# Kernel optimization log

Measured on AMD Instinct MI355X. Metric: run time of the kernel, lower is better.

## Reference

```python
import jax, jax.numpy as jnp
import numpy as np
import math

B, T, N, D = 2, 128, 64, 128
H = 8
DK = D // H
DE = 32
LW = 8
CLIP_MIN, CLIP_MAX = -5.0, 5.0


def setup_inputs() -> dict:
    key = jax.random.key(0)
    ks = jax.random.split(key, 12)
    node = jax.random.normal(ks[0], (B, T, N, D), jnp.float32)
    tv = jax.random.normal(ks[1], (B, N, T, T, DE), jnp.float32)
    mask = jax.random.randint(ks[2], (B, 1, T), 0, 2, jnp.int32)
    # banded local mask |i-j| <= LW
    idx = jnp.arange(T)
    local_mask = (jnp.abs(idx[:, None] - idx[None, :]) <= LW).astype(jnp.float32)
    s = 0.02
    W_qkv = jax.random.normal(ks[3], (D, 3 * D), jnp.float32) * s
    b_qkv = jnp.zeros((3 * D,), jnp.float32)
    W_g = jax.random.normal(ks[4], (DE, H), jnp.float32) * s
    b_g = jnp.zeros((H,), jnp.float32)
    W_out = jax.random.normal(ks[5], (D, D), jnp.float32) * s
    b_out = jnp.zeros((D,), jnp.float32)
    W_upd = jax.random.normal(ks[6], (H, DE), jnp.float32) * s
    b_upd = jnp.zeros((DE,), jnp.float32)
    return {"node": node, "tv": tv, "mask": mask, "local_mask": local_mask,
            "W_qkv": W_qkv, "b_qkv": b_qkv, "W_g": W_g, "b_g": b_g,
            "W_out": W_out, "b_out": b_out, "W_upd": W_upd, "b_upd": b_upd}


def reference(node, tv, mask, local_mask, W_qkv, b_qkv, W_g, b_g, W_out, b_out, W_upd, b_upd):
    # node: (B,T,N,D) -> (B*N, T, D)  (einops '(b n) t d' ordering: index b*N+n)
    x = node.transpose(0, 2, 1, 3).reshape(B * N, T, D)
    qkv = x @ W_qkv + b_qkv                              # (BN, T, 3D)
    qkv = qkv.reshape(B * N, T, H, DK, 3)                # grouped (h, d_k, 3)
    q = qkv[..., 0].transpose(0, 2, 1, 3)                # (BN, H, T, DK)
    k = qkv[..., 1].transpose(0, 2, 1, 3)
    v = qkv[..., 2].transpose(0, 2, 1, 3)
    # edge-conditioned bias g: (BN, T, T, DE) -> (BN, H, T, T)
    g = (tv.reshape(B * N, T, T, DE) @ W_g + b_g).transpose(0, 3, 1, 2)
    scores = jnp.einsum('bhtd,bhsd->bhts', q, k) / math.sqrt(DK)
    scores = scores + g * local_mask                     # banded edge bias
    scores = jnp.clip(scores, CLIP_MIN, CLIP_MAX)
    m = jnp.repeat(mask, N, axis=0)[:, None]             # (BN,1,1,T)
    scores = jnp.where(m == 0, jnp.float32(1e-28), scores)
    attn = jax.nn.softmax(scores, axis=-1)
    attn = jnp.where(m == 0, jnp.float32(0.0), attn)
    xo = jnp.einsum('bhts,bhsd->bhtd', attn, v)          # (BN,H,T,DK)
    xo = xo.transpose(0, 2, 1, 3).reshape(B, N, T, D).transpose(0, 2, 1, 3)  # (B,T,N,D)
    xo = xo @ W_out + b_out
    sc = scores.reshape(B, N, H, T, T).transpose(0, 1, 3, 4, 2)  # (B,N,T,T,H)
    tv_out = sc @ W_upd + b_upd                          # (B,N,T,T,DE)
    return (xo, tv_out)
```

## Files before the change

### kernel.cpp

```cpp
#include <hip/hip_runtime.h>
#include <math.h>

#define BB 2
#define TT 128
#define NN 64
#define DD 128
#define HH 8
#define DKK 16
#define DEE 32
#define LWW 8
#define BNN (BB*NN)

typedef float floatx4 __attribute__((ext_vector_type(4)));

__global__ __launch_bounds__(256) void qkv_kernel(
    const float* __restrict__ node, const float* __restrict__ Wqkv,
    const float* __restrict__ bqkv,
    float* __restrict__ Q, float* __restrict__ K, float* __restrict__ V) {
  __shared__ float xs[32 * 128];
  __shared__ float wl[16 * 384];
  const int tid = threadIdx.x;
  const int row0 = blockIdx.x * 32;

  for (int i4 = tid; i4 < 1024; i4 += 256) {
    int r = i4 >> 5, d4 = i4 & 31;
    int rowg = row0 + r;
    int bn = rowg >> 7, t = rowg & 127;
    int b = bn >> 6, n = bn & 63;
    float4 v = *(const float4*)&node[(((size_t)(b * TT + t)) * NN + n) * DD + d4 * 4];
    *(float4*)&xs[r * 128 + d4 * 4] = v;
  }

  float acc[48];
#pragma unroll
  for (int i = 0; i < 48; ++i) acc[i] = 0.f;
  const int tr = tid >> 5;
  const int tc = tid & 31;

  for (int ct = 0; ct < 8; ++ct) {
    __syncthreads();
    for (int i4 = tid; i4 < 1536; i4 += 256) {
      int c = i4 / 96, j4 = i4 % 96;
      *(float4*)&wl[c * 384 + j4 * 4] =
          *(const float4*)&Wqkv[(size_t)(ct * 16 + c) * 384 + j4 * 4];
    }
    __syncthreads();
#pragma unroll
    for (int cl4 = 0; cl4 < 4; ++cl4) {
      floatx4 xr[4];
#pragma unroll
      for (int i = 0; i < 4; ++i)
        xr[i] = *(const floatx4*)&xs[(tr * 4 + i) * 128 + ct * 16 + cl4 * 4];
#pragma unroll
      for (int jj = 0; jj < 4; ++jj) {
        const float* wp = &wl[(cl4 * 4 + jj) * 384 + tc * 12];
        floatx4 w0 = *(const floatx4*)&wp[0];
        floatx4 w1 = *(const floatx4*)&wp[4];
        floatx4 w2 = *(const floatx4*)&wp[8];
#pragma unroll
        for (int i = 0; i < 4; ++i) {
          float x = xr[i][jj];
          acc[i * 12 + 0] += x * w0[0];  acc[i * 12 + 1] += x * w0[1];
          acc[i * 12 + 2] += x * w0[2];  acc[i * 12 + 3] += x * w0[3];
          acc[i * 12 + 4] += x * w1[0];  acc[i * 12 + 5] += x * w1[1];
          acc[i * 12 + 6] += x * w1[2];  acc[i * 12 + 7] += x * w1[3];
          acc[i * 12 + 8] += x * w2[0];  acc[i * 12 + 9] += x * w2[1];
          acc[i * 12 +10] += x * w2[2];  acc[i * 12 +11] += x * w2[3];
        }
      }
    }
  }

  const int h = tc >> 2;
  const int dk0 = (tc & 3) * 4;
#pragma unroll
  for (int i = 0; i < 4; ++i) {
    int rowg = row0 + tr * 4 + i;
    int bn = rowg >> 7, t = rowg & 127;
    float qv[4], kv[4], vv[4];
#pragma unroll
    for (int dl = 0; dl < 4; ++dl) {
      int jb = h * 48 + (dk0 + dl) * 3;
      qv[dl] = acc[i * 12 + dl * 3 + 0] + bqkv[jb + 0];
      kv[dl] = acc[i * 12 + dl * 3 + 1] + bqkv[jb + 1];
      vv[dl] = acc[i * 12 + dl * 3 + 2] + bqkv[jb + 2];
    }
    *(float4*)&Q[(size_t)rowg * 128 + h * 16 + dk0] = *(float4*)qv;
    *(float4*)&K[(((size_t)(bn * 8 + h)) * 128 + t) * 16 + dk0] = *(float4*)kv;
#pragma unroll
    for (int dl = 0; dl < 4; ++dl)
      V[(((size_t)(bn * 8 + h)) * 16 + dk0 + dl) * 128 + t] = vv[dl];
  }
}

__global__ __launch_bounds__(256) void attn_kernel(
    const float* __restrict__ Q, const float* __restrict__ K,
    const float* __restrict__ V, const float* __restrict__ tv,
    const int* __restrict__ mask,
    const float* __restrict__ Wg, const float* __restrict__ bg,
    const float* __restrict__ Wout, const float* __restrict__ bout,
    const float* __restrict__ Wupd, const float* __restrict__ bupd,
    float* __restrict__ out0, float* __restrict__ out1) {
  __shared__ float sc[8 * 8 * 128];
  __shared__ float qs[8 * 128];
  __shared__ float swg[DEE * HH];
  __shared__ float swu[HH * DEE];
  __shared__ float sbg[HH];
  __shared__ float sbu[DEE];
  __shared__ int smask[TT];

  const int tid = threadIdx.x;
  const int xcd = blockIdx.x & 7;
  const int i = blockIdx.x >> 3;
  const int bn = xcd * 16 + (i & 15);
  const int t0 = (i >> 4) * 8;
  const int b = bn >> 6, n = bn & 63;

  swg[tid & 255] = Wg[tid & 255];
  swu[tid & 255] = Wupd[tid & 255];
  if (tid < DEE) sbu[tid] = bupd[tid];
  if (tid < HH) sbg[tid] = bg[tid];
  if (tid < TT) smask[tid] = mask[b * TT + tid];
  __syncthreads();

  {
    const int h = tid >> 5;
    const int s4 = tid & 31;
    const floatx4* kp =
        (const floatx4*)&K[(((size_t)(bn * 8 + h)) * 128 + s4 * 4) * 16];
    floatx4 kr[16];
#pragma unroll
    for (int u = 0; u < 16; ++u) kr[u] = kp[u];
    int m[4];
#pragma unroll
    for (int j = 0; j < 4; ++j) m[j] = smask[s4 * 4 + j];
#pragma unroll
    for (int t8 = 0; t8 < 8; ++t8) {
      const floatx4* qp =
          (const floatx4*)&Q[((size_t)(bn * TT + t0 + t8)) * 128 + h * 16];
      floatx4 q0 = qp[0], q1 = qp[1], q2 = qp[2], q3 = qp[3];
      const int t = t0 + t8;
      floatx4 res;
#pragma unroll
      for (int j = 0; j < 4; ++j) {
        floatx4 p = q0 * kr[j * 4 + 0];
        p += q1 * kr[j * 4 + 1];
        p += q2 * kr[j * 4 + 2];
        p += q3 * kr[j * 4 + 3];
        float v = (p[0] + p[1] + p[2] + p[3]) * 0.25f;
        int s = s4 * 4 + j;
        bool inband = (s >= t - LWW) && (s <= t + LWW);
        if (!inband) {
          v = fminf(fmaxf(v, -5.f), 5.f);
          if (m[j] == 0) v = 1e-28f;
        }
        res[j] = v;
      }
      *(floatx4*)&sc[(t8 * 8 + h) * 128 + s4 * 4] = res;
    }
  }
  __syncthreads();

  if (tid < 8 * (2 * LWW + 1)) {
    int t8 = tid / 17, ds = tid % 17;
    int t = t0 + t8, s = t - LWW + ds;
    if (s >= 0 && s < TT) {
      const float4* tp = (const float4*)&tv[(((size_t)(bn * TT + t)) * TT + s) * DEE];
      float gh[HH];
#pragma unroll
      for (int h = 0; h < HH; ++h) gh[h] = sbg[h];
#pragma unroll
      for (int c4 = 0; c4 < 8; ++c4) {
        float4 tvv = tp[c4];
#pragma unroll
        for (int h = 0; h < HH; ++h) {
          gh[h] += tvv.x * swg[(c4 * 4 + 0) * 8 + h] +
                   tvv.y * swg[(c4 * 4 + 1) * 8 + h] +
                   tvv.z * swg[(c4 * 4 + 2) * 8 + h] +
                   tvv.w * swg[(c4 * 4 + 3) * 8 + h];
        }
      }
      int m0 = smask[s];
#pragma unroll
      for (int h = 0; h < HH; ++h) {
        float v = sc[(t8 * 8 + h) * 128 + s] + gh[h];
        v = fminf(fmaxf(v, -5.f), 5.f);
        if (m0 == 0) v = 1e-28f;
        sc[(t8 * 8 + h) * 128 + s] = v;
      }
    }
  }
  __syncthreads();

  {
    const int e4 = tid & 7;
    const int sq = tid >> 3;
    floatx4 wv[HH];
#pragma unroll
    for (int h = 0; h < HH; ++h) wv[h] = *(const floatx4*)&swu[h * 32 + e4 * 4];
    floatx4 bu = *(const floatx4*)&sbu[e4 * 4];
    for (int t8 = 0; t8 < 8; ++t8) {
      float* op = out1 + (((size_t)(bn * TT + t0 + t8)) * TT) * DEE;
      floatx4 o0 = bu, o1 = bu, o2 = bu, o3 = bu;
#pragma unroll
      for (int h = 0; h < HH; ++h) {
        floatx4 f = *(const floatx4*)&sc[(t8 * 8 + h) * 128 + sq * 4];
        o0 += f[0] * wv[h];
        o1 += f[1] * wv[h];
        o2 += f[2] * wv[h];
        o3 += f[3] * wv[h];
      }
      __builtin_nontemporal_store(o0, (floatx4*)&op[(sq * 4 + 0) * DEE + e4 * 4]);
      __builtin_nontemporal_store(o1, (floatx4*)&op[(sq * 4 + 1) * DEE + e4 * 4]);
      __builtin_nontemporal_store(o2, (floatx4*)&op[(sq * 4 + 2) * DEE + e4 * 4]);
      __builtin_nontemporal_store(o3, (floatx4*)&op[(sq * 4 + 3) * DEE + e4 * 4]);
    }
  }
  __syncthreads();

  {
    const int l = tid & 31;
    const int rsub = tid >> 5;
#pragma unroll
    for (int p = 0; p < 8; ++p) {
      int row = p * 8 + rsub;
      float* r = &sc[row * 128];
      float x0 = r[l], x1 = r[l + 32], x2 = r[l + 64], x3 = r[l + 96];
      float m = fmaxf(fmaxf(x0, x1), fmaxf(x2, x3));
      m = fmaxf(m, __shfl_xor(m, 1));
      m = fmaxf(m, __shfl_xor(m, 2));
      m = fmaxf(m, __shfl_xor(m, 4));
      m = fmaxf(m, __shfl_xor(m, 8));
      m = fmaxf(m, __shfl_xor(m, 16));
      float e0 = __expf(x0 - m), e1 = __expf(x1 - m),
            e2 = __expf(x2 - m), e3 = __expf(x3 - m);
      float ssum = e0 + e1 + e2 + e3;
      ssum += __shfl_xor(ssum, 1);
      ssum += __shfl_xor(ssum, 2);
      ssum += __shfl_xor(ssum, 4);
      ssum += __shfl_xor(ssum, 8);
      ssum += __shfl_xor(ssum, 16);
      float inv = 1.f / ssum;
      r[l]      = (smask[l]      == 0) ? 0.f : e0 * inv;
      r[l + 32] = (smask[l + 32] == 0) ? 0.f : e1 * inv;
      r[l + 64] = (smask[l + 64] == 0) ? 0.f : e2 * inv;
      r[l + 96] = (smask[l + 96] == 0) ? 0.f : e3 * inv;
    }
  }
  __syncthreads();

  {
    const int dk4 = tid & 3;
    const int h = (tid >> 2) & 7;
    const int t8 = tid >> 5;
    const int rr = (t8 * 8 + h) & 31;
    const floatx4* ap = (const floatx4*)&sc[(t8 * 8 + h) * 128];
    const floatx4* vp0 =
        (const floatx4*)&V[(((size_t)(bn * 8 + h)) * 16 + dk4 * 4 + 0) * 128];
    const floatx4* vp1 =
        (const floatx4*)&V[(((size_t)(bn * 8 + h)) * 16 + dk4 * 4 + 1) * 128];
    const floatx4* vp2 =
        (const floatx4*)&V[(((size_t)(bn * 8 + h)) * 16 + dk4 * 4 + 2) * 128];
    const floatx4* vp3 =
        (const floatx4*)&V[(((size_t)(bn * 8 + h)) * 16 + dk4 * 4 + 3) * 128];
    floatx4 a0 = 0.f, a1 = 0.f, a2 = 0.f, a3 = 0.f;
#pragma unroll 8
    for (int it = 0; it < 32; ++it) {
      int s4 = (it + rr) & 31;
      floatx4 av = ap[s4];
      a0 += av * vp0[s4];
      a1 += av * vp1[s4];
      a2 += av * vp2[s4];
      a3 += av * vp3[s4];
    }
    floatx4 r;
    r[0] = a0[0] + a0[1] + a0[2] + a0[3];
    r[1] = a1[0] + a1[1] + a1[2] + a1[3];
    r[2] = a2[0] + a2[1] + a2[2] + a2[3];
    r[3] = a3[0] + a3[1] + a3[2] + a3[3];
    *(floatx4*)&qs[t8 * 128 + h * 16 + dk4 * 4] = r;
  }
  __syncthreads();

  {
    const int d = tid & 127, tg = tid >> 7;
    float bo = bout[d];
    float accp[4] = {bo, bo, bo, bo};
    for (int c4 = 0; c4 < 32; ++c4) {
      floatx4 x0 = *(const floatx4*)&qs[(tg * 4 + 0) * 128 + c4 * 4];
      floatx4 x1 = *(const floatx4*)&qs[(tg * 4 + 1) * 128 + c4 * 4];
      floatx4 x2 = *(const floatx4*)&qs[(tg * 4 + 2) * 128 + c4 * 4];
      floatx4 x3 = *(const floatx4*)&qs[(tg * 4 + 3) * 128 + c4 * 4];
      const float* wp = &Wout[(size_t)(c4 * 4) * 128 + d];
      float w0 = wp[0], w1 = wp[128], w2 = wp[256], w3 = wp[384];
      accp[0] += x0[0] * w0 + x0[1] * w1 + x0[2] * w2 + x0[3] * w3;
      accp[1] += x1[0] * w0 + x1[1] * w1 + x1[2] * w2 + x1[3] * w3;
      accp[2] += x2[0] * w0 + x2[1] * w1 + x2[2] * w2 + x2[3] * w3;
      accp[3] += x3[0] * w0 + x3[1] * w1 + x3[2] * w2 + x3[3] * w3;
    }
#pragma unroll
    for (int u = 0; u < 4; ++u) {
      int t = t0 + tg * 4 + u;
      __builtin_nontemporal_store(accp[u],
          &out0[(((size_t)(b * TT + t)) * NN + n) * DD + d]);
    }
  }
}

extern "C" void kernel_launch(void* const* d_in, const int* in_sizes, int n_in,
                              void* d_out, int out_size, void* d_ws, size_t ws_size,
                              hipStream_t stream) {
  const float* node = (const float*)d_in[0];
  const float* tv   = (const float*)d_in[1];
  const int*   mask = (const int*)d_in[2];
  const float* Wqkv = (const float*)d_in[4];
  const float* bqkv = (const float*)d_in[5];
  const float* Wg   = (const float*)d_in[6];
  const float* bg   = (const float*)d_in[7];
  const float* Wout = (const float*)d_in[8];
  const float* bout = (const float*)d_in[9];
  const float* Wupd = (const float*)d_in[10];
  const float* bupd = (const float*)d_in[11];

  float* out0 = (float*)d_out;
  float* out1 = out0 + (size_t)BB * TT * NN * DD;

  float* Q = (float*)d_ws;
  float* K = Q + (size_t)BNN * TT * DD;
  float* V = K + (size_t)BNN * TT * DD;

  qkv_kernel<<<512, 256, 0, stream>>>(node, Wqkv, bqkv, Q, K, V);
  attn_kernel<<<2048, 256, 0, stream>>>(Q, K, V, tv, mask, Wg, bg, Wout, bout,
                                        Wupd, bupd, out0, out1);
}
```

Before: 636.8 us.

## Make attention stages wave-local and halve QKV tile rows

The attention kernel now gives each 64-lane wave two query rows for every stage after score computation, so block-wide __syncthreads become wave barriers. Shared copies of the small weights and the mask are dropped in favour of direct global loads. The score buffer gets a padded stride to avoid LDS bank conflicts, and the output projection uses vectorized Wout loads with a cross-half shuffle reduction. The QKV kernel processes 16 rows per block and launches twice as many blocks, trading weight-tile reuse for more parallelism and fewer registers.

```diff
diff --git a/kernel.cpp b/kernel.cpp
--- a/kernel.cpp
+++ b/kernel.cpp
@@ -10,6 +10,7 @@
 #define DEE 32
 #define LWW 8
 #define BNN (BB*NN)
+#define SCP 132
 
 typedef float floatx4 __attribute__((ext_vector_type(4)));
 
@@ -17,23 +18,23 @@
     const float* __restrict__ node, const float* __restrict__ Wqkv,
     const float* __restrict__ bqkv,
     float* __restrict__ Q, float* __restrict__ K, float* __restrict__ V) {
-  __shared__ float xs[32 * 128];
+  __shared__ float xs[16 * 128];
   __shared__ float wl[16 * 384];
   const int tid = threadIdx.x;
-  const int row0 = blockIdx.x * 32;
-
-  for (int i4 = tid; i4 < 1024; i4 += 256) {
+  const int row0 = blockIdx.x * 16;
+
+  for (int i4 = tid; i4 < 512; i4 += 256) {
     int r = i4 >> 5, d4 = i4 & 31;
     int rowg = row0 + r;
     int bn = rowg >> 7, t = rowg & 127;
     int b = bn >> 6, n = bn & 63;
-    float4 v = *(const float4*)&node[(((size_t)(b * TT + t)) * NN + n) * DD + d4 * 4];
-    *(float4*)&xs[r * 128 + d4 * 4] = v;
-  }
-
-  float acc[48];
-#pragma unroll
-  for (int i = 0; i < 48; ++i) acc[i] = 0.f;
+    *(float4*)&xs[r * 128 + d4 * 4] =
+        *(const float4*)&node[(((size_t)(b * TT + t)) * NN + n) * DD + d4 * 4];
+  }
+
+  float acc[24];
+#pragma unroll
+  for (int i = 0; i < 24; ++i) acc[i] = 0.f;
   const int tr = tid >> 5;
   const int tc = tid & 31;
 
@@ -47,10 +48,10 @@
     __syncthreads();
 #pragma unroll
     for (int cl4 = 0; cl4 < 4; ++cl4) {
-      floatx4 xr[4];
-#pragma unroll
-      for (int i = 0; i < 4; ++i)
-        xr[i] = *(const floatx4*)&xs[(tr * 4 + i) * 128 + ct * 16 + cl4 * 4];
+      floatx4 xr[2];
+#pragma unroll
+      for (int i = 0; i < 2; ++i)
+        xr[i] = *(const floatx4*)&xs[(tr * 2 + i) * 128 + ct * 16 + cl4 * 4];
 #pragma unroll
       for (int jj = 0; jj < 4; ++jj) {
         const float* wp = &wl[(cl4 * 4 + jj) * 384 + tc * 12];
@@ -58,7 +59,7 @@
         floatx4 w1 = *(const floatx4*)&wp[4];
         floatx4 w2 = *(const floatx4*)&wp[8];
 #pragma unroll
-        for (int i = 0; i < 4; ++i) {
+        for (int i = 0; i < 2; ++i) {
           float x = xr[i][jj];
           acc[i * 12 + 0] += x * w0[0];  acc[i * 12 + 1] += x * w0[1];
           acc[i * 12 + 2] += x * w0[2];  acc[i * 12 + 3] += x * w0[3];
@@ -74,8 +75,8 @@
   const int h = tc >> 2;
   const int dk0 = (tc & 3) * 4;
 #pragma unroll
-  for (int i = 0; i < 4; ++i) {
-    int rowg = row0 + tr * 4 + i;
+  for (int i = 0; i < 2; ++i) {
+    int rowg = row0 + tr * 2 + i;
     int bn = rowg >> 7, t = rowg & 127;
     float qv[4], kv[4], vv[4];
 #pragma unroll
@@ -101,13 +102,8 @@
     const float* __restrict__ Wout, const float* __restrict__ bout,
     const float* __restrict__ Wupd, const float* __restrict__ bupd,
     float* __restrict__ out0, float* __restrict__ out1) {
-  __shared__ float sc[8 * 8 * 128];
-  __shared__ float qs[8 * 128];
-  __shared__ float swg[DEE * HH];
-  __shared__ float swu[HH * DEE];
-  __shared__ float sbg[HH];
-  __shared__ float sbu[DEE];
-  __shared__ int smask[TT];
+  __shared__ float sc[64 * SCP];
+  __shared__ float xo[4][2][128];
 
   const int tid = threadIdx.x;
   const int xcd = blockIdx.x & 7;
@@ -116,13 +112,6 @@
   const int t0 = (i >> 4) * 8;
   const int b = bn >> 6, n = bn & 63;
 
-  swg[tid & 255] = Wg[tid & 255];
-  swu[tid & 255] = Wupd[tid & 255];
-  if (tid < DEE) sbu[tid] = bupd[tid];
-  if (tid < HH) sbg[tid] = bg[tid];
-  if (tid < TT) smask[tid] = mask[b * TT + tid];
-  __syncthreads();
-
   {
     const int h = tid >> 5;
     const int s4 = tid & 31;
@@ -131,9 +120,8 @@
     floatx4 kr[16];
 #pragma unroll
     for (int u = 0; u < 16; ++u) kr[u] = kp[u];
-    int m[4];
-#pragma unroll
-    for (int j = 0; j < 4; ++j) m[j] = smask[s4 * 4 + j];
+    int4 mi = *(const int4*)&mask[b * TT + s4 * 4];
+    int m[4] = {mi.x, mi.y, mi.z, mi.w};
 #pragma unroll
     for (int t8 = 0; t8 < 8; ++t8) {
       const floatx4* qp =
@@ -156,154 +144,187 @@
         }
         res[j] = v;
       }
-      *(floatx4*)&sc[(t8 * 8 + h) * 128 + s4 * 4] = res;
+      *(floatx4*)&sc[(t8 * 8 + h) * SCP + s4 * 4] = res;
     }
   }
   __syncthreads();
 
-  if (tid < 8 * (2 * LWW + 1)) {
-    int t8 = tid / 17, ds = tid % 17;
-    int t = t0 + t8, s = t - LWW + ds;
+  const int wid = tid >> 6, lane = tid & 63;
+  const int tw0 = t0 + wid * 2;
+  float* scw = &sc[(wid * 2) * 8 * SCP];
+
+  if (lane < 34) {
+    const int r = lane / 17, ds = lane - r * 17;
+    const int t = tw0 + r, s = t - LWW + ds;
     if (s >= 0 && s < TT) {
-      const float4* tp = (const float4*)&tv[(((size_t)(bn * TT + t)) * TT + s) * DEE];
-      float gh[HH];
-#pragma unroll
-      for (int h = 0; h < HH; ++h) gh[h] = sbg[h];
+      const floatx4* tp =
+          (const floatx4*)&tv[(((size_t)(bn * TT + t)) * TT + s) * DEE];
+      floatx4 glo = *(const floatx4*)&bg[0];
+      floatx4 ghi = *(const floatx4*)&bg[4];
 #pragma unroll
       for (int c4 = 0; c4 < 8; ++c4) {
-        float4 tvv = tp[c4];
-#pragma unroll
-        for (int h = 0; h < HH; ++h) {
-          gh[h] += tvv.x * swg[(c4 * 4 + 0) * 8 + h] +
-                   tvv.y * swg[(c4 * 4 + 1) * 8 + h] +
-                   tvv.z * swg[(c4 * 4 + 2) * 8 + h] +
-                   tvv.w * swg[(c4 * 4 + 3) * 8 + h];
+        floatx4 tvv = tp[c4];
+#pragma unroll
+        for (int k = 0; k < 4; ++k) {
+          floatx4 wlo = *(const floatx4*)&Wg[(c4 * 4 + k) * 8];
+          floatx4 whi = *(const floatx4*)&Wg[(c4 * 4 + k) * 8 + 4];
+          glo += tvv[k] * wlo;
+          ghi += tvv[k] * whi;
         }
       }
-      int m0 = smask[s];
-#pragma unroll
-      for (int h = 0; h < HH; ++h) {
-        float v = sc[(t8 * 8 + h) * 128 + s] + gh[h];
+      int m0 = mask[b * TT + s];
+      float* base = &scw[r * 8 * SCP + s];
+#pragma unroll
+      for (int h = 0; h < 8; ++h) {
+        float gv = (h < 4) ? glo[h] : ghi[h - 4];
+        float v = base[h * SCP] + gv;
         v = fminf(fmaxf(v, -5.f), 5.f);
         if (m0 == 0) v = 1e-28f;
-        sc[(t8 * 8 + h) * 128 + s] = v;
-      }
-    }
-  }
-  __syncthreads();
-
-  {
-    const int e4 = tid & 7;
-    const int sq = tid >> 3;
+        base[h * SCP] = v;
+      }
+    }
+  }
+  __builtin_amdgcn_wave_barrier();
+
+  {
+    const int e4 = lane & 7;
+    const int sq0 = lane >> 3;
     floatx4 wv[HH];
 #pragma unroll
-    for (int h = 0; h < HH; ++h) wv[h] = *(const floatx4*)&swu[h * 32 + e4 * 4];
-    floatx4 bu = *(const floatx4*)&sbu[e4 * 4];
-    for (int t8 = 0; t8 < 8; ++t8) {
-      float* op = out1 + (((size_t)(bn * TT + t0 + t8)) * TT) * DEE;
-      floatx4 o0 = bu, o1 = bu, o2 = bu, o3 = bu;
-#pragma unroll
-      for (int h = 0; h < HH; ++h) {
-        floatx4 f = *(const floatx4*)&sc[(t8 * 8 + h) * 128 + sq * 4];
-        o0 += f[0] * wv[h];
-        o1 += f[1] * wv[h];
-        o2 += f[2] * wv[h];
-        o3 += f[3] * wv[h];
-      }
-      __builtin_nontemporal_store(o0, (floatx4*)&op[(sq * 4 + 0) * DEE + e4 * 4]);
-      __builtin_nontemporal_store(o1, (floatx4*)&op[(sq * 4 + 1) * DEE + e4 * 4]);
-      __builtin_nontemporal_store(o2, (floatx4*)&op[(sq * 4 + 2) * DEE + e4 * 4]);
-      __builtin_nontemporal_store(o3, (floatx4*)&op[(sq * 4 + 3) * DEE + e4 * 4]);
-    }
-  }
-  __syncthreads();
-
-  {
-    const int l = tid & 31;
-    const int rsub = tid >> 5;
-#pragma unroll
-    for (int p = 0; p < 8; ++p) {
-      int row = p * 8 + rsub;
-      float* r = &sc[row * 128];
-      float x0 = r[l], x1 = r[l + 32], x2 = r[l + 64], x3 = r[l + 96];
-      float m = fmaxf(fmaxf(x0, x1), fmaxf(x2, x3));
+    for (int h = 0; h < HH; ++h) wv[h] = *(const floatx4*)&Wupd[h * 32 + e4 * 4];
+    floatx4 bu = *(const floatx4*)&bupd[e4 * 4];
+#pragma unroll
+    for (int r = 0; r < 2; ++r) {
+      const float* scr = &scw[r * 8 * SCP];
+      float* op = out1 + ((size_t)(bn * TT + tw0 + r)) * TT * DEE;
+#pragma unroll
+      for (int si = 0; si < 4; ++si) {
+        int sq = sq0 + si * 8;
+        floatx4 o0 = bu, o1 = bu, o2 = bu, o3 = bu;
+#pragma unroll
+        for (int h = 0; h < HH; ++h) {
+          floatx4 f = *(const floatx4*)&scr[h * SCP + sq * 4];
+          o0 += f[0] * wv[h];
+          o1 += f[1] * wv[h];
+          o2 += f[2] * wv[h];
+          o3 += f[3] * wv[h];
+        }
+        __builtin_nontemporal_store(o0, (floatx4*)&op[(sq * 4 + 0) * DEE + e4 * 4]);
+        __builtin_nontemporal_store(o1, (floatx4*)&op[(sq * 4 + 1) * DEE + e4 * 4]);
+        __builtin_nontemporal_store(o2, (floatx4*)&op[(sq * 4 + 2) * DEE + e4 * 4]);
+        __builtin_nontemporal_store(o3, (floatx4*)&op[(sq * 4 + 3) * DEE + e4 * 4]);
+      }
+    }
+  }
+  __builtin_amdgcn_wave_barrier();
+
+  {
+    const int h = lane >> 3, sp = lane & 7;
+    int4 mi0 = *(const int4*)&mask[b * TT + sp * 4];
+    int4 mi1 = *(const int4*)&mask[b * TT + sp * 4 + 32];
+    int4 mi2 = *(const int4*)&mask[b * TT + sp * 4 + 64];
+    int4 mi3 = *(const int4*)&mask[b * TT + sp * 4 + 96];
+#pragma unroll
+    for (int r = 0; r < 2; ++r) {
+      float* rp = &scw[(r * 8 + h) * SCP];
+      floatx4 x0 = *(const floatx4*)&rp[sp * 4];
+      floatx4 x1 = *(const floatx4*)&rp[sp * 4 + 32];
+      floatx4 x2 = *(const floatx4*)&rp[sp * 4 + 64];
+      floatx4 x3 = *(const floatx4*)&rp[sp * 4 + 96];
+      float m = fmaxf(fmaxf(fmaxf(x0[0], x0[1]), fmaxf(x0[2], x0[3])),
+                      fmaxf(fmaxf(x1[0], x1[1]), fmaxf(x1[2], x1[3])));
+      m = fmaxf(m, fmaxf(fmaxf(fmaxf(x2[0], x2[1]), fmaxf(x2[2], x2[3])),
+                         fmaxf(fmaxf(x3[0], x3[1]), fmaxf(x3[2], x3[3]))));
       m = fmaxf(m, __shfl_xor(m, 1));
       m = fmaxf(m, __shfl_xor(m, 2));
       m = fmaxf(m, __shfl_xor(m, 4));
-      m = fmaxf(m, __shfl_xor(m, 8));
-      m = fmaxf(m, __shfl_xor(m, 16));
-      float e0 = __expf(x0 - m), e1 = __expf(x1 - m),
-            e2 = __expf(x2 - m), e3 = __expf(x3 - m);
-      float ssum = e0 + e1 + e2 + e3;
+      floatx4 e0, e1, e2, e3;
+#pragma unroll
+      for (int j = 0; j < 4; ++j) {
+        e0[j] = __expf(x0[j] - m);
+        e1[j] = __expf(x1[j] - m);
+        e2[j] = __expf(x2[j] - m);
+        e3[j] = __expf(x3[j] - m);
+      }
+      float ssum = (e0[0] + e0[1] + e0[2] + e0[3]) + (e1[0] + e1[1] + e1[2] + e1[3]) +
+                   (e2[0] + e2[1] + e2[2] + e2[3]) + (e3[0] + e3[1] + e3[2] + e3[3]);
       ssum += __shfl_xor(ssum, 1);
       ssum += __shfl_xor(ssum, 2);
       ssum += __shfl_xor(ssum, 4);
-      ssum += __shfl_xor(ssum, 8);
-      ssum += __shfl_xor(ssum, 16);
       float inv = 1.f / ssum;
-      r[l]      = (smask[l]      == 0) ? 0.f : e0 * inv;
-      r[l + 32] = (smask[l + 32] == 0) ? 0.f : e1 * inv;
-      r[l + 64] = (smask[l + 64] == 0) ? 0.f : e2 * inv;
-      r[l + 96] = (smask[l + 96] == 0) ? 0.f : e3 * inv;
-    }
-  }
-  __syncthreads();
-
-  {
-    const int dk4 = tid & 3;
-    const int h = (tid >> 2) & 7;
-    const int t8 = tid >> 5;
-    const int rr = (t8 * 8 + h) & 31;
-    const floatx4* ap = (const floatx4*)&sc[(t8 * 8 + h) * 128];
+      floatx4 y0, y1, y2, y3;
+      y0[0] = (mi0.x == 0) ? 0.f : e0[0] * inv;
+      y0[1] = (mi0.y == 0) ? 0.f : e0[1] * inv;
+      y0[2] = (mi0.z == 0) ? 0.f : e0[2] * inv;
+      y0[3] = (mi0.w == 0) ? 0.f : e0[3] * inv;
+      y1[0] = (mi1.x == 0) ? 0.f : e1[0] * inv;
+      y1[1] = (mi1.y == 0) ? 0.f : e1[1] * inv;
+      y1[2] = (mi1.z == 0) ? 0.f : e1[2] * inv;
+      y1[3] = (mi1.w == 0) ? 0.f : e1[3] * inv;
+      y2[0] = (mi2.x == 0) ? 0.f : e2[0] * inv;
+      y2[1] = (mi2.y == 0) ? 0.f : e2[1] * inv;
+      y2[2] = (mi2.z == 0) ? 0.f : e2[2] * inv;
+      y2[3] = (mi2.w == 0) ? 0.f : e2[3] * inv;
+      y3[0] = (mi3.x == 0) ? 0.f : e3[0] * inv;
+      y3[1] = (mi3.y == 0) ? 0.f : e3[1] * inv;
+      y3[2] = (mi3.z == 0) ? 0.f : e3[2] * inv;
+      y3[3] = (mi3.w == 0) ? 0.f : e3[3] * inv;
+      *(floatx4*)&rp[sp * 4]      = y0;
+      *(floatx4*)&rp[sp * 4 + 32] = y1;
+      *(floatx4*)&rp[sp * 4 + 64] = y2;
+      *(floatx4*)&rp[sp * 4 + 96] = y3;
+    }
+  }
+  __builtin_amdgcn_wave_barrier();
+
+  {
+    const int h = lane >> 3, dk2 = lane & 7;
     const floatx4* vp0 =
-        (const floatx4*)&V[(((size_t)(bn * 8 + h)) * 16 + dk4 * 4 + 0) * 128];
+        (const floatx4*)&V[(((size_t)(bn * 8 + h)) * 16 + dk2) * 128];
     const floatx4* vp1 =
-        (const floatx4*)&V[(((size_t)(bn * 8 + h)) * 16 + dk4 * 4 + 1) * 128];
-    const floatx4* vp2 =
-        (const floatx4*)&V[(((size_t)(bn * 8 + h)) * 16 + dk4 * 4 + 2) * 128];
-    const floatx4* vp3 =
-        (const floatx4*)&V[(((size_t)(bn * 8 + h)) * 16 + dk4 * 4 + 3) * 128];
-    floatx4 a0 = 0.f, a1 = 0.f, a2 = 0.f, a3 = 0.f;
+        (const floatx4*)&V[(((size_t)(bn * 8 + h)) * 16 + dk2 + 8) * 128];
+    const floatx4* ap0 = (const floatx4*)&scw[(0 * 8 + h) * SCP];
+    const floatx4* ap1 = (const floatx4*)&scw[(1 * 8 + h) * SCP];
+    floatx4 a00 = 0.f, a01 = 0.f, a10 = 0.f, a11 = 0.f;
+#pragma unroll 4
+    for (int s4 = 0; s4 < 32; ++s4) {
+      floatx4 v0 = vp0[s4], v1 = vp1[s4];
+      floatx4 p0 = ap0[s4], p1 = ap1[s4];
+      a00 += p0 * v0;
+      a01 += p0 * v1;
+      a10 += p1 * v0;
+      a11 += p1 * v1;
+    }
+    float* xw = &xo[wid][0][0];
+    xw[h * 16 + dk2]           = a00[0] + a00[1] + a00[2] + a00[3];
+    xw[h * 16 + dk2 + 8]       = a01[0] + a01[1] + a01[2] + a01[3];
+    xw[128 + h * 16 + dk2]     = a10[0] + a10[1] + a10[2] + a10[3];
+    xw[128 + h * 16 + dk2 + 8] = a11[0] + a11[1] + a11[2] + a11[3];
+  }
+  __builtin_amdgcn_wave_barrier();
+
+  {
+    const int d4 = lane & 31, ch = lane >> 5;
+    const float* xp0 = &xo[wid][0][0];
+    const float* xp1 = &xo[wid][1][0];
+    floatx4 acc0 = 0.f, acc1 = 0.f;
 #pragma unroll 8
-    for (int it = 0; it < 32; ++it) {
-      int s4 = (it + rr) & 31;
-      floatx4 av = ap[s4];
-      a0 += av * vp0[s4];
-      a1 += av * vp1[s4];
-      a2 += av * vp2[s4];
-      a3 += av * vp3[s4];
-    }
-    floatx4 r;
-    r[0] = a0[0] + a0[1] + a0[2] + a0[3];
-    r[1] = a1[0] + a1[1] + a1[2] + a1[3];
-    r[2] = a2[0] + a2[1] + a2[2] + a2[3];
-    r[3] = a3[0] + a3[1] + a3[2] + a3[3];
-    *(floatx4*)&qs[t8 * 128 + h * 16 + dk4 * 4] = r;
-  }
-  __syncthreads();
-
-  {
-    const int d = tid & 127, tg = tid >> 7;
-    float bo = bout[d];
-    float accp[4] = {bo, bo, bo, bo};
-    for (int c4 = 0; c4 < 32; ++c4) {
-      floatx4 x0 = *(const floatx4*)&qs[(tg * 4 + 0) * 128 + c4 * 4];
-      floatx4 x1 = *(const floatx4*)&qs[(tg * 4 + 1) * 128 + c4 * 4];
-      floatx4 x2 = *(const floatx4*)&qs[(tg * 4 + 2) * 128 + c4 * 4];
-      floatx4 x3 = *(const floatx4*)&qs[(tg * 4 + 3) * 128 + c4 * 4];
-      const float* wp = &Wout[(size_t)(c4 * 4) * 128 + d];
-      float w0 = wp[0], w1 = wp[128], w2 = wp[256], w3 = wp[384];
-      accp[0] += x0[0] * w0 + x0[1] * w1 + x0[2] * w2 + x0[3] * w3;
-      accp[1] += x1[0] * w0 + x1[1] * w1 + x1[2] * w2 + x1[3] * w3;
-      accp[2] += x2[0] * w0 + x2[1] * w1 + x2[2] * w2 + x2[3] * w3;
-      accp[3] += x3[0] * w0 + x3[1] * w1 + x3[2] * w2 + x3[3] * w3;
-    }
-#pragma unroll
-    for (int u = 0; u < 4; ++u) {
-      int t = t0 + tg * 4 + u;
-      __builtin_nontemporal_store(accp[u],
-          &out0[(((size_t)(b * TT + t)) * NN + n) * DD + d]);
-    }
+    for (int ci = 0; ci < 64; ++ci) {
+      int c = ch * 64 + ci;
+      floatx4 w = *(const floatx4*)&Wout[(size_t)c * 128 + d4 * 4];
+      acc0 += xp0[c] * w;
+      acc1 += xp1[c] * w;
+    }
+#pragma unroll
+    for (int j = 0; j < 4; ++j) {
+      acc0[j] += __shfl_xor(acc0[j], 32);
+      acc1[j] += __shfl_xor(acc1[j], 32);
+    }
+    floatx4 bo = *(const floatx4*)&bout[d4 * 4];
+    floatx4 res = (ch == 0 ? acc0 : acc1) + bo;
+    int t = tw0 + ch;
+    __builtin_nontemporal_store(res,
+        (floatx4*)&out0[(((size_t)(b * TT + t)) * NN + n) * DD + d4 * 4]);
   }
 }
 
@@ -329,7 +350,7 @@
   float* K = Q + (size_t)BNN * TT * DD;
   float* V = K + (size_t)BNN * TT * DD;
 
-  qkv_kernel<<<512, 256, 0, stream>>>(node, Wqkv, bqkv, Q, K, V);
+  qkv_kernel<<<1024, 256, 0, stream>>>(node, Wqkv, bqkv, Q, K, V);
   attn_kernel<<<2048, 256, 0, stream>>>(Q, K, V, tv, mask, Wg, bg, Wout, bout,
                                         Wupd, bupd, out0, out1);
 }
```

Measured after the change: 550.8 us. 1.16x faster.
